# Optimization experiments

Measured on AMD Instinct MI355X. Metric: run time of the kernel, lower is better.

## Reference

```python
import jax, jax.numpy as jnp
import numpy as np
from jax import lax

B, C, H, W = 16, 512, 16, 300
K, G = 8, 2          # k_clusters, g_clusters (gvlad)
OUT = 5994           # n speakers
DN = ('NCHW', 'OIHW', 'NCHW')


def setup_inputs() -> dict:
    key = jax.random.key(0)
    ks = jax.random.split(key, 10)
    s = lambda fan: 1.0 / np.sqrt(fan)
    return {
        'x5': jax.random.normal(ks[0], (B, C, H, W), jnp.float32),
        'x4': jnp.zeros((1, 1, 1, 1), jnp.float32),
        'x3': jnp.zeros((1, 1, 1, 1), jnp.float32),
        'x2': jnp.zeros((1, 1, 1, 1), jnp.float32),
        'x1': jnp.zeros((1, 1, 1, 1), jnp.float32),
        'conv_w': jax.random.normal(ks[1], (C, C, 7, 1), jnp.float32) * s(C * 7),
        'conv_b': jnp.zeros((C,), jnp.float32),
        'cc_w': jax.random.normal(ks[2], (K + G, C, 7, 1), jnp.float32) * s(C * 7),
        'cc_b': jnp.zeros((K + G,), jnp.float32),
        'centroids': jax.random.normal(ks[3], (K + G, C), jnp.float32),
        'fc_w': jax.random.normal(ks[4], (C, C * K), jnp.float32) * s(C * K),
        'fc_b': jnp.zeros((C,), jnp.float32),
        'logit_w': jax.random.normal(ks[5], (OUT, C), jnp.float32) * s(C),
    }


def _conv(x, w, b=None):
    y = lax.conv_general_dilated(x, w, (1, 1), 'VALID', dimension_numbers=DN)
    if b is not None:
        y = y + b[None, :, None, None]
    return y


def _forward(x5, conv_w, conv_b, cc_w, cc_b, centroids, fc_w, fc_b, logit_w):
    feats = jnp.maximum(_conv(x5, conv_w, conv_b), 0.0)      # (B,C,H',W) relu conv
    scores = _conv(x5, cc_w, cc_b)                           # (B,K+G,H',W)
    assign = jax.nn.softmax(scores, axis=1)                  # soft cluster assignment
    # VLAD: sum_hw a[b,k,h,w]*(f[b,c,h,w] - cent[k,c]), computed without
    # materializing the (B,K+G,C,H',W) residual tensor (same math, fused form)
    agg = jnp.einsum('bkhw,bchw->bkc', assign, feats)        # (B,K+G,C)
    asum = jnp.sum(assign, axis=(2, 3))                      # (B,K+G)
    cluster_res = agg - asum[:, :, None] * centroids[None]   # (B,K+G,C)
    cluster_res = cluster_res[:, :K, :]                      # gvlad: drop ghost clusters
    norm = jnp.linalg.norm(cluster_res, axis=-1, keepdims=True)
    cluster_l2 = cluster_res / jnp.maximum(norm, 1e-12)
    vlad = cluster_l2.reshape(-1, K * C)                     # (B, K*C)
    emb = jnp.maximum(vlad @ fc_w.T + fc_b, 0.0)             # (B,C)
    logit = emb @ logit_w.T                                  # (B,OUT)
    return emb, logit


def reference(x5, x4, x3, x2, x1, conv_w, conv_b, cc_w, cc_b, centroids,
              fc_w, fc_b, logit_w):
    # x4..x1 are unused by Decoder.forward (only x5 flows through)
    return _forward(x5, conv_w, conv_b, cc_w, cc_b, centroids, fc_w, fc_b, logit_w)
```

## Files before the change

kernel.cpp:

```cpp
#include <hip/hip_runtime.h>
#include <hip/hip_bf16.h>

typedef __attribute__((ext_vector_type(8))) short bf16x8;
typedef __attribute__((ext_vector_type(4))) float f32x4;

__device__ __forceinline__ void async16(const void* g, void* l) {
    __builtin_amdgcn_global_load_lds(
        (const __attribute__((address_space(1))) unsigned int*)g,
        (__attribute__((address_space(3))) unsigned int*)l, 16, 0, 0);
}

__global__ __launch_bounds__(256) void pack_all(const float* __restrict__ x5,
                                                const float* __restrict__ conv_w,
                                                const float* __restrict__ cc_w,
                                                __hip_bfloat16* __restrict__ X3,
                                                __hip_bfloat16* __restrict__ A2f) {
    __shared__ __align__(16) float smem[64 * 65];
    const int f = blockIdx.x;
    if (f < 10240) {
        float(*tile)[65] = (float(*)[65])smem;
        const int ct = f / 1280, r = f % 1280;
        const int wt = r >> 8, bh = r & 255;
        const int b = bh >> 4, h = bh & 15;
        const int w0 = wt * 64, c0 = ct * 64;
        const int lw = (threadIdx.x & 15) * 4;
        const int lc = threadIdx.x >> 4;
#pragma unroll
        for (int i = 0; i < 4; ++i) {
            const int c = lc + i * 16;
            const int w = w0 + lw;
            const float* src = &x5[((size_t)(b * 512 + c0 + c) * 16 + h) * 300 + w];
            float4 v = {0.f, 0.f, 0.f, 0.f};
            if (w + 3 < 300) v = *(const float4*)src;
            else {
                if (w < 300)     v.x = src[0];
                if (w + 1 < 300) v.y = src[1];
                if (w + 2 < 300) v.z = src[2];
            }
            *(float4*)&tile[c][lw] = v;
        }
        __syncthreads();
        const int sc = (threadIdx.x & 7) * 8;
        const int sw0 = threadIdx.x >> 3;
#pragma unroll
        for (int i = 0; i < 2; ++i) {
            const int wl = sw0 + i * 32;
            const int w = w0 + wl;
            if (w < 300) {
                __hip_bfloat16 p[8];
#pragma unroll
                for (int j = 0; j < 8; ++j) p[j] = __float2bfloat16(tile[sc + j][wl]);
                *(uint4*)&X3[(((size_t)(b * 16 + h) * 300 + w)) * 512 + c0 + sc] = *(uint4*)p;
            }
        }
    } else {
        float* w = smem;
        const int co = f - 10240;
        if (co < 522) {
            const float4* src = (co < 512) ? (const float4*)(conv_w + (size_t)co * 3584)
                                           : (const float4*)(cc_w + (size_t)(co - 512) * 3584);
            for (int i = threadIdx.x; i < 896; i += 256) *(float4*)&w[i * 4] = src[i];
        } else {
            for (int i = threadIdx.x; i < 3584; i += 256) w[i] = 0.f;
        }
        __syncthreads();
        const int g = co >> 4, fl = co & 15;
        for (int chunk = threadIdx.x; chunk < 448; chunk += 256) {
            const int kk0 = chunk * 8;
            const int kt = kk0 >> 5, sq = (kk0 >> 3) & 3;
            __hip_bfloat16 p[8];
#pragma unroll
            for (int j = 0; j < 8; ++j) {
                const int k = kk0 + j;
                p[j] = __float2bfloat16(w[(k & 511) * 7 + (k >> 9)]);
            }
            char* dst = (char*)A2f + (((size_t)g * 112 + kt) * 64 + sq * 16 + fl) * 16;
            *(uint4*)dst = *(uint4*)p;
        }
    }
}

__global__ __launch_bounds__(256) void scores_gemm(
    const __hip_bfloat16* __restrict__ A2f, const __hip_bfloat16* __restrict__ X3,
    const float* __restrict__ cc_b, float* __restrict__ assign,
    float* __restrict__ asum_part, float* __restrict__ agg) {
    __shared__ __align__(16) char lds[65536];
    __shared__ float sred[4][4][4];
    const int tid = threadIdx.x;
    const int wv = tid >> 6;
    const int lane = tid & 63;
    const int gid = blockIdx.x;
    const int xcd = gid & 7;
    const int j = gid >> 3;
    const int b = xcd * 2 + (j >= 12 ? 1 : 0);
    const int nt2 = j % 12;

    {
        const int base = gid * 427;
        for (int i = tid; i < 427; i += 256) {
            const int idx = base + i;
            if (idx < 81920) agg[idx] = 0.f;
        }
    }

    const int row0 = wv * 16 + (lane >> 2);
    const int kseg = (lane & 3) ^ ((lane >> 3) & 3);
    const char* gB[4];
#pragma unroll
    for (int q = 0; q < 4; ++q) {
        int n = nt2 * 256 + row0 + q * 64;
        if (n > 2999) n = 2999;
        gB[q] = (const char*)X3 + ((size_t)((b * 16 + n / 300) * 300 + n % 300)) * 1024 + (size_t)kseg * 16;
    }
    char* lB = lds + wv * 1024 + lane * 16;

    const int wn = wv * 64;
    const int fl = lane & 15;
    const int sq = lane >> 4;
    int boff[4];
#pragma unroll
    for (int i = 0; i < 4; ++i) {
        const int swz = (sq ^ ((fl >> 1) & 3)) * 16;
        boff[i] = (wn + i * 16 + fl) * 64 + swz;
    }
    const char* Af = (const char*)A2f + (((size_t)32 * 112) << 10) + (lane << 4);

    f32x4 acc[4] = {};
    bf16x8 aC[2], aN[2];

#define S_ISSUE(ktp, ph)                                                               \
    {                                                                                  \
        const int kt0 = (ktp) * 2;                                                     \
        const size_t ba0 = (size_t)(kt0 >> 4) * 307200 + (size_t)(kt0 & 15) * 64;      \
        const size_t ba1 = (size_t)((kt0 + 1) >> 4) * 307200 + (size_t)((kt0 + 1) & 15) * 64; \
        _Pragma("unroll")                                                              \
        for (int q = 0; q < 4; ++q) {                                                  \
            async16(gB[q] + ba0, lB + (ph) * 32768 + q * 4096);                        \
            async16(gB[q] + ba1, lB + (ph) * 32768 + 16384 + q * 4096);                \
        }                                                                              \
    }
#define S_PREA(ktp, arr)                                                               \
    {                                                                                  \
        arr[0] = *(const bf16x8*)(Af + ((size_t)((ktp) * 2) << 10));                   \
        arr[1] = *(const bf16x8*)(Af + ((size_t)((ktp) * 2 + 1) << 10));               \
    }
#define S_COMP(ph, arr)                                                                \
    {                                                                                  \
        _Pragma("unroll")                                                              \
        for (int kk = 0; kk < 2; ++kk) {                                               \
            _Pragma("unroll")                                                          \
            for (int ni = 0; ni < 4; ++ni) {                                           \
                const bf16x8 bv = *(const bf16x8*)(lds + (ph) * 32768 + kk * 16384 + boff[ni]); \
                acc[ni] = __builtin_amdgcn_mfma_f32_16x16x32_bf16(arr[kk], bv, acc[ni], 0, 0, 0); \
            }                                                                          \
        }                                                                              \
    }

    S_ISSUE(0, 0);
    S_PREA(0, aC);
    for (int ktp = 0; ktp < 56; ktp += 2) {
        __syncthreads();
        S_ISSUE(ktp + 1, 1);
        S_PREA(ktp + 1, aN);
        S_COMP(0, aC);
        __syncthreads();
        if (ktp < 54) { S_ISSUE(ktp + 2, 0); S_PREA(ktp + 2, aC); }
        S_COMP(1, aN);
    }
#undef S_ISSUE
#undef S_PREA
#undef S_COMP

    float pa[4] = {0.f, 0.f, 0.f, 0.f};
#pragma unroll
    for (int ni = 0; ni < 4; ++ni) {
        const int n = nt2 * 256 + wn + ni * 16 + fl;
        const bool nval = (n < 3000);
        float s[4];
#pragma unroll
        for (int r = 0; r < 4; ++r) {
            const int k = sq * 4 + r;
            s[r] = (k < 10) ? (acc[ni][r] + cc_b[k]) : -1e30f;
        }
        float mx = fmaxf(fmaxf(s[0], s[1]), fmaxf(s[2], s[3]));
        mx = fmaxf(mx, __shfl_xor(mx, 16, 64));
        mx = fmaxf(mx, __shfl_xor(mx, 32, 64));
        float e[4], es = 0.f;
#pragma unroll
        for (int r = 0; r < 4; ++r) {
            e[r] = (sq * 4 + r < 10) ? __expf(s[r] - mx) : 0.f;
            es += e[r];
        }
        es += __shfl_xor(es, 16, 64);
        es += __shfl_xor(es, 32, 64);
        const float inv = 1.f / es;
#pragma unroll
        for (int r = 0; r < 4; ++r) {
            const int k = sq * 4 + r;
            const float a = e[r] * inv;
            if (nval) {
                if (k < 10) assign[(size_t)(b * 10 + k) * 3000 + n] = a;
                pa[r] += a;
            }
        }
    }
#pragma unroll
    for (int off = 1; off < 16; off <<= 1)
#pragma unroll
        for (int r = 0; r < 4; ++r) pa[r] += __shfl_xor(pa[r], off, 64);
    if (fl == 0) {
#pragma unroll
        for (int r = 0; r < 4; ++r) sred[wv][sq][r] = pa[r];
    }
    __syncthreads();
    if (tid < 10)
        asum_part[(nt2 * 16 + b) * 10 + tid] =
            sred[0][tid >> 2][tid & 3] + sred[1][tid >> 2][tid & 3] +
            sred[2][tid >> 2][tid & 3] + sred[3][tid >> 2][tid & 3];
}

__global__ __launch_bounds__(256, 4) void conv_gemm(
    const __hip_bfloat16* __restrict__ A2f, const __hip_bfloat16* __restrict__ X3,
    const float* __restrict__ conv_b, const float* __restrict__ assign,
    float* __restrict__ agg) {
    __shared__ __align__(16) char lds[16384];
    const int tid = threadIdx.x;
    const int wv = tid >> 6;
    const int lane = tid & 63;

    const int gid = blockIdx.x;
    const int xcd = gid & 7;
    const int j = gid >> 3;
    const int nb = xcd * 48 + (j >> 2);
    const int m0 = (j & 3) * 128;
    const int b = nb / 24;
    const int nt = nb % 24;

    const int row0 = wv * 16 + (lane >> 2);
    const int kseg = (lane & 3) ^ ((lane >> 3) & 3);
    int n0 = nt * 128 + row0;      if (n0 > 2999) n0 = 2999;
    int n1 = nt * 128 + row0 + 64; if (n1 > 2999) n1 = 2999;
    const char* gB0 = (const char*)X3 + ((size_t)((b * 16 + n0 / 300) * 300 + n0 % 300)) * 1024 + (size_t)kseg * 16;
    const char* gB1 = (const char*)X3 + ((size_t)((b * 16 + n1 / 300) * 300 + n1 % 300)) * 1024 + (size_t)kseg * 16;
    char* lB = lds + wv * 1024 + lane * 16;

    const int wm = (wv & 1) * 64;
    const int wn = (wv >> 1) * 64;
    const int fl = lane & 15;
    const int sq = lane >> 4;
    int boff[4];
#pragma unroll
    for (int i = 0; i < 4; ++i) {
        const int swz = (sq ^ ((fl >> 1) & 3)) * 16;
        boff[i] = (wn + i * 16 + fl) * 64 + swz;
    }
    const char* Af = (const char*)A2f;
    const int gb = (m0 >> 4) + ((wv & 1) << 2);

    f32x4 acc[4][4] = {};
    bf16x8 aC[4], aN[4];

#define ISSUE_B(kt, ph)                                                                \
    {                                                                                  \
        const size_t badd = (size_t)((kt) >> 4) * 307200 + (size_t)((kt) & 15) * 64;   \
        async16(gB0 + badd, lB + (ph) * 8192);                                         \
        async16(gB1 + badd, lB + (ph) * 8192 + 4096);                                  \
    }
#define PRE_A(kt, arr)                                                                 \
    {                                                                                  \
        _Pragma("unroll")                                                              \
        for (int mi = 0; mi < 4; ++mi)                                                 \
            arr[mi] = *(const bf16x8*)(Af + (((size_t)(gb + mi) * 112 + (kt)) << 10) + (lane << 4)); \
    }
#define COMPUTE(ph, arr)                                                               \
    {                                                                                  \
        _Pragma("unroll")                                                              \
        for (int ni = 0; ni < 4; ++ni) {                                               \
            const bf16x8 bv = *(const bf16x8*)(lds + (ph) * 8192 + boff[ni]);          \
            _Pragma("unroll")                                                          \
            for (int mi = 0; mi < 4; ++mi)                                             \
                acc[mi][ni] = __builtin_amdgcn_mfma_f32_16x16x32_bf16(arr[mi], bv, acc[mi][ni], 0, 0, 0); \
        }                                                                              \
    }

    ISSUE_B(0, 0);
    PRE_A(0, aC);
    for (int kt = 0; kt < 112; kt += 2) {
        __syncthreads();
        ISSUE_B(kt + 1, 1);
        PRE_A(kt + 1, aN);
        COMPUTE(0, aC);
        __syncthreads();
        if (kt < 110) { ISSUE_B(kt + 2, 0); PRE_A(kt + 2, aC); }
        COMPUTE(1, aN);
    }
#undef ISSUE_B
#undef PRE_A
#undef COMPUTE

    const int quad4 = sq * 4;
#pragma unroll
    for (int mi = 0; mi < 4; ++mi) {
        const int cob = m0 + wm + mi * 16 + quad4;
        const float b0 = conv_b[cob + 0], b1 = conv_b[cob + 1],
                    b2 = conv_b[cob + 2], b3 = conv_b[cob + 3];
#pragma unroll
        for (int ni = 0; ni < 4; ++ni) {
            acc[mi][ni][0] = fmaxf(acc[mi][ni][0] + b0, 0.f);
            acc[mi][ni][1] = fmaxf(acc[mi][ni][1] + b1, 0.f);
            acc[mi][ni][2] = fmaxf(acc[mi][ni][2] + b2, 0.f);
            acc[mi][ni][3] = fmaxf(acc[mi][ni][3] + b3, 0.f);
        }
    }
    int nn[4];
#pragma unroll
    for (int ni = 0; ni < 4; ++ni) nn[ni] = nt * 128 + wn + ni * 16 + fl;
    const float* asg = assign + (size_t)b * 30000;
    for (int k = 0; k < 10; ++k) {
        float av[4];
#pragma unroll
        for (int ni = 0; ni < 4; ++ni)
            av[ni] = (nn[ni] < 3000) ? asg[(size_t)k * 3000 + nn[ni]] : 0.f;
        float part[16];
#pragma unroll
        for (int mi = 0; mi < 4; ++mi)
#pragma unroll
            for (int r = 0; r < 4; ++r)
                part[mi * 4 + r] = av[0] * acc[mi][0][r] + av[1] * acc[mi][1][r]
                                 + av[2] * acc[mi][2][r] + av[3] * acc[mi][3][r];
#pragma unroll
        for (int off = 1; off < 16; off <<= 1)
#pragma unroll
            for (int i = 0; i < 16; ++i)
                part[i] += __shfl_xor(part[i], off, 64);
        if (fl == 0) {
            float* ag = agg + (size_t)(b * 10 + k) * 512;
#pragma unroll
            for (int mi = 0; mi < 4; ++mi)
#pragma unroll
                for (int r = 0; r < 4; ++r)
                    atomicAdd(&ag[m0 + wm + mi * 16 + quad4 + r], part[mi * 4 + r]);
        }
    }
}

__global__ __launch_bounds__(256) void fc_fused(const float* __restrict__ agg,
                                                const float* __restrict__ asum_part,
                                                const float* __restrict__ centroids,
                                                const float* __restrict__ fc_w,
                                                const float* __restrict__ fc_b,
                                                float* __restrict__ out) {
    __shared__ float res[4096];
    __shared__ float sasum[8];
    __shared__ float red[4][8];
    __shared__ float scale[8];
    const int b = blockIdx.y;
    const int t = threadIdx.x;
    if (t < 8) {
        float s = 0.f;
#pragma unroll
        for (int p = 0; p < 12; ++p) s += asum_part[(p * 16 + b) * 10 + t];
        sasum[t] = s;
    }
    __syncthreads();
    float sq[8];
#pragma unroll
    for (int k = 0; k < 8; ++k) sq[k] = 0.f;
#pragma unroll
    for (int jj = 0; jj < 16; ++jj) {
        const int i = t + jj * 256;
        const int k = jj >> 1;
        const int c = i & 511;
        const float r = agg[(size_t)(b * 10 + k) * 512 + c] - sasum[k] * centroids[k * 512 + c];
        res[i] = r;
        sq[k] += r * r;
    }
    const int lane = t & 63, w = t >> 6;
#pragma unroll
    for (int k = 0; k < 8; ++k) {
        float v = sq[k];
        for (int off = 32; off; off >>= 1) v += __shfl_xor(v, off, 64);
        if (lane == 0) red[w][k] = v;
    }
    __syncthreads();
    if (t < 8) {
        const float nrm = sqrtf(red[0][t] + red[1][t] + red[2][t] + red[3][t]);
        scale[t] = 1.f / fmaxf(nrm, 1e-12f);
    }
    __syncthreads();

    const int col = t >> 3;
    const int ks = t & 7;
    const int co = blockIdx.x * 32 + col;
    const float4* w4 = (const float4*)(fc_w + (size_t)co * 4096);
    float acc = 0.f;
    for (int i = ks; i < 1024; i += 8) {
        const float4 wv = w4[i];
        const float4 rv = *(const float4*)&res[i * 4];
        acc += (rv.x * wv.x + rv.y * wv.y + rv.z * wv.z + rv.w * wv.w) * scale[i >> 7];
    }
    acc += __shfl_down(acc, 4, 8);
    acc += __shfl_down(acc, 2, 8);
    acc += __shfl_down(acc, 1, 8);
    if (ks == 0) out[b * 512 + co] = fmaxf(acc + fc_b[co], 0.f);
}

__global__ __launch_bounds__(256) void logit_kernel(const float* __restrict__ emb,
                                                    const float* __restrict__ logit_w,
                                                    float* __restrict__ out) {
    __shared__ float se[512];
    const int gid = blockIdx.x;
    const int xcd = gid & 7;
    const int j = gid >> 3;
    const int otile = xcd * 3 + (j >> 4);
    const int b = j & 15;
    se[threadIdx.x] = emb[b * 512 + threadIdx.x];
    se[threadIdx.x + 256] = emb[b * 512 + threadIdx.x + 256];
    __syncthreads();
    const int o = otile * 256 + threadIdx.x;
    if (o < 5994) {
        const float4* w4 = (const float4*)(logit_w + (size_t)o * 512);
        float acc = 0.f;
        for (int i = 0; i < 128; ++i) {
            const float4 w = w4[i];
            acc += w.x * se[4 * i] + w.y * se[4 * i + 1] + w.z * se[4 * i + 2] + w.w * se[4 * i + 3];
        }
        out[8192 + b * 5994 + o] = acc;
    }
}

extern "C" void kernel_launch(void* const* d_in, const int* in_sizes, int n_in,
                              void* d_out, int out_size, void* d_ws, size_t ws_size,
                              hipStream_t stream) {
    (void)in_sizes; (void)n_in; (void)out_size; (void)ws_size;
    const float* x5       = (const float*)d_in[0];
    const float* conv_w   = (const float*)d_in[5];
    const float* conv_b   = (const float*)d_in[6];
    const float* cc_w     = (const float*)d_in[7];
    const float* cc_b     = (const float*)d_in[8];
    const float* centroids= (const float*)d_in[9];
    const float* fc_w     = (const float*)d_in[10];
    const float* fc_b     = (const float*)d_in[11];
    const float* logit_w  = (const float*)d_in[12];
    float* out = (float*)d_out;

    char* ws = (char*)d_ws;
    __hip_bfloat16* X3  = (__hip_bfloat16*)(ws);
    __hip_bfloat16* A2f = (__hip_bfloat16*)(ws + 78643200);
    float* assign       = (float*)(ws + 83230720);
    float* asum_part    = (float*)(ws + 85150720);
    float* agg          = (float*)(ws + 85158400);

    pack_all<<<dim3(10880), 256, 0, stream>>>(x5, conv_w, cc_w, X3, A2f);
    scores_gemm<<<dim3(192), 256, 0, stream>>>(A2f, X3, cc_b, assign, asum_part, agg);
    conv_gemm<<<dim3(1536), 256, 0, stream>>>(A2f, X3, conv_b, assign, agg);
    fc_fused<<<dim3(16, 16), 256, 0, stream>>>(agg, asum_part, centroids, fc_w, fc_b, out);
    logit_kernel<<<dim3(384), 256, 0, stream>>>(out, logit_w, out);
}
```

Measured before the change: 652.2 us.

## Shrink scores GEMM tiles to 64 columns and use a transpose-reduce for agg

The scores GEMM now runs 768 blocks of 64 columns instead of 192 blocks of 256. Each wave computes one 16x16 MFMA tile and reads its operands straight from global memory, with no LDS staging or double buffering. The aim is more parallelism across CUs for this small-K-output GEMM, at the cost of losing data reuse through LDS. In conv_gemm, the per-cluster 16-value butterfly reduction becomes a recursive-halving transpose-reduce, so each lane ends up holding one output. The two wave-halves are then combined through LDS, which cuts shuffles and atomics by a factor of two or more; asum_part and the workspace offsets are resized to match.

```diff
diff --git a/kernel.cpp b/kernel.cpp
--- a/kernel.cpp
+++ b/kernel.cpp
@@ -84,125 +84,65 @@
     const __hip_bfloat16* __restrict__ A2f, const __hip_bfloat16* __restrict__ X3,
     const float* __restrict__ cc_b, float* __restrict__ assign,
     float* __restrict__ asum_part, float* __restrict__ agg) {
-    __shared__ __align__(16) char lds[65536];
     __shared__ float sred[4][4][4];
     const int tid = threadIdx.x;
     const int wv = tid >> 6;
     const int lane = tid & 63;
+    const int fl = lane & 15;
+    const int sq = lane >> 4;
     const int gid = blockIdx.x;
     const int xcd = gid & 7;
     const int j = gid >> 3;
-    const int b = xcd * 2 + (j >= 12 ? 1 : 0);
-    const int nt2 = j % 12;
+    const int b = xcd * 2 + (j >= 48 ? 1 : 0);
+    const int nt = j % 48;
 
     {
-        const int base = gid * 427;
-        for (int i = tid; i < 427; i += 256) {
+        const int base = gid * 107;
+        for (int i = tid; i < 107; i += 256) {
             const int idx = base + i;
             if (idx < 81920) agg[idx] = 0.f;
         }
     }
 
-    const int row0 = wv * 16 + (lane >> 2);
-    const int kseg = (lane & 3) ^ ((lane >> 3) & 3);
-    const char* gB[4];
-#pragma unroll
-    for (int q = 0; q < 4; ++q) {
-        int n = nt2 * 256 + row0 + q * 64;
-        if (n > 2999) n = 2999;
-        gB[q] = (const char*)X3 + ((size_t)((b * 16 + n / 300) * 300 + n % 300)) * 1024 + (size_t)kseg * 16;
-    }
-    char* lB = lds + wv * 1024 + lane * 16;
-
-    const int wn = wv * 64;
-    const int fl = lane & 15;
-    const int sq = lane >> 4;
-    int boff[4];
-#pragma unroll
-    for (int i = 0; i < 4; ++i) {
-        const int swz = (sq ^ ((fl >> 1) & 3)) * 16;
-        boff[i] = (wn + i * 16 + fl) * 64 + swz;
-    }
-    const char* Af = (const char*)A2f + (((size_t)32 * 112) << 10) + (lane << 4);
-
-    f32x4 acc[4] = {};
-    bf16x8 aC[2], aN[2];
-
-#define S_ISSUE(ktp, ph)                                                               \
-    {                                                                                  \
-        const int kt0 = (ktp) * 2;                                                     \
-        const size_t ba0 = (size_t)(kt0 >> 4) * 307200 + (size_t)(kt0 & 15) * 64;      \
-        const size_t ba1 = (size_t)((kt0 + 1) >> 4) * 307200 + (size_t)((kt0 + 1) & 15) * 64; \
-        _Pragma("unroll")                                                              \
-        for (int q = 0; q < 4; ++q) {                                                  \
-            async16(gB[q] + ba0, lB + (ph) * 32768 + q * 4096);                        \
-            async16(gB[q] + ba1, lB + (ph) * 32768 + 16384 + q * 4096);                \
-        }                                                                              \
-    }
-#define S_PREA(ktp, arr)                                                               \
-    {                                                                                  \
-        arr[0] = *(const bf16x8*)(Af + ((size_t)((ktp) * 2) << 10));                   \
-        arr[1] = *(const bf16x8*)(Af + ((size_t)((ktp) * 2 + 1) << 10));               \
-    }
-#define S_COMP(ph, arr)                                                                \
-    {                                                                                  \
-        _Pragma("unroll")                                                              \
-        for (int kk = 0; kk < 2; ++kk) {                                               \
-            _Pragma("unroll")                                                          \
-            for (int ni = 0; ni < 4; ++ni) {                                           \
-                const bf16x8 bv = *(const bf16x8*)(lds + (ph) * 32768 + kk * 16384 + boff[ni]); \
-                acc[ni] = __builtin_amdgcn_mfma_f32_16x16x32_bf16(arr[kk], bv, acc[ni], 0, 0, 0); \
-            }                                                                          \
-        }                                                                              \
-    }
-
-    S_ISSUE(0, 0);
-    S_PREA(0, aC);
-    for (int ktp = 0; ktp < 56; ktp += 2) {
-        __syncthreads();
-        S_ISSUE(ktp + 1, 1);
-        S_PREA(ktp + 1, aN);
-        S_COMP(0, aC);
-        __syncthreads();
-        if (ktp < 54) { S_ISSUE(ktp + 2, 0); S_PREA(ktp + 2, aC); }
-        S_COMP(1, aN);
-    }
-#undef S_ISSUE
-#undef S_PREA
-#undef S_COMP
-
-    float pa[4] = {0.f, 0.f, 0.f, 0.f};
-#pragma unroll
-    for (int ni = 0; ni < 4; ++ni) {
-        const int n = nt2 * 256 + wn + ni * 16 + fl;
-        const bool nval = (n < 3000);
-        float s[4];
-#pragma unroll
-        for (int r = 0; r < 4; ++r) {
-            const int k = sq * 4 + r;
-            s[r] = (k < 10) ? (acc[ni][r] + cc_b[k]) : -1e30f;
-        }
-        float mx = fmaxf(fmaxf(s[0], s[1]), fmaxf(s[2], s[3]));
-        mx = fmaxf(mx, __shfl_xor(mx, 16, 64));
-        mx = fmaxf(mx, __shfl_xor(mx, 32, 64));
-        float e[4], es = 0.f;
-#pragma unroll
-        for (int r = 0; r < 4; ++r) {
-            e[r] = (sq * 4 + r < 10) ? __expf(s[r] - mx) : 0.f;
-            es += e[r];
-        }
-        es += __shfl_xor(es, 16, 64);
-        es += __shfl_xor(es, 32, 64);
-        const float inv = 1.f / es;
-#pragma unroll
-        for (int r = 0; r < 4; ++r) {
-            const int k = sq * 4 + r;
-            const float a = e[r] * inv;
-            if (nval) {
-                if (k < 10) assign[(size_t)(b * 10 + k) * 3000 + n] = a;
-                pa[r] += a;
-            }
-        }
+    const int n = nt * 64 + wv * 16 + fl;
+    const int nc = n > 2999 ? 2999 : n;
+    const char* gB = (const char*)X3 + ((size_t)(b * 4800 + nc)) * 1024 + sq * 16;
+    const char* Af = (const char*)A2f + (((size_t)32 * 112) << 10) + ((size_t)lane << 4);
+
+    f32x4 acc = {};
+#pragma unroll 4
+    for (int kt = 0; kt < 112; ++kt) {
+        const bf16x8 a  = *(const bf16x8*)(Af + ((size_t)kt << 10));
+        const bf16x8 bv = *(const bf16x8*)(gB + (size_t)(kt >> 4) * 307200 + (size_t)(kt & 15) * 64);
+        acc = __builtin_amdgcn_mfma_f32_16x16x32_bf16(a, bv, acc, 0, 0, 0);
+    }
+
+    float s[4];
+#pragma unroll
+    for (int r = 0; r < 4; ++r) {
+        const int k = sq * 4 + r;
+        s[r] = (k < 10) ? (acc[r] + cc_b[k]) : -1e30f;
+    }
+    float mx = fmaxf(fmaxf(s[0], s[1]), fmaxf(s[2], s[3]));
+    mx = fmaxf(mx, __shfl_xor(mx, 16, 64));
+    mx = fmaxf(mx, __shfl_xor(mx, 32, 64));
+    float e[4], es = 0.f;
+#pragma unroll
+    for (int r = 0; r < 4; ++r) {
+        e[r] = (sq * 4 + r < 10) ? __expf(s[r] - mx) : 0.f;
+        es += e[r];
+    }
+    es += __shfl_xor(es, 16, 64);
+    es += __shfl_xor(es, 32, 64);
+    const float inv = 1.f / es;
+    const bool nval = (n < 3000);
+    float pa[4];
+#pragma unroll
+    for (int r = 0; r < 4; ++r) {
+        const int k = sq * 4 + r;
+        const float a = e[r] * inv;
+        pa[r] = nval ? a : 0.f;
+        if (nval && k < 10) assign[(size_t)(b * 10 + k) * 3000 + n] = a;
     }
 #pragma unroll
     for (int off = 1; off < 16; off <<= 1)
@@ -214,7 +154,7 @@
     }
     __syncthreads();
     if (tid < 10)
-        asum_part[(nt2 * 16 + b) * 10 + tid] =
+        asum_part[(nt * 16 + b) * 10 + tid] =
             sred[0][tid >> 2][tid & 3] + sred[1][tid >> 2][tid & 3] +
             sred[2][tid >> 2][tid & 3] + sred[3][tid >> 2][tid & 3];
 }
@@ -316,6 +256,9 @@
 #pragma unroll
     for (int ni = 0; ni < 4; ++ni) nn[ni] = nt * 128 + wn + ni * 16 + fl;
     const float* asg = assign + (size_t)b * 30000;
+    const int s_ = ((fl & 1) << 3) | ((fl & 2) << 1) | ((fl & 4) >> 1) | ((fl & 8) >> 3);
+    const int co_off = (s_ >> 2) * 16 + quad4 + (s_ & 3);
+    float red10[10];
     for (int k = 0; k < 10; ++k) {
         float av[4];
 #pragma unroll
@@ -329,17 +272,31 @@
                 part[mi * 4 + r] = av[0] * acc[mi][0][r] + av[1] * acc[mi][1][r]
                                  + av[2] * acc[mi][2][r] + av[3] * acc[mi][3][r];
 #pragma unroll
-        for (int off = 1; off < 16; off <<= 1)
-#pragma unroll
-            for (int i = 0; i < 16; ++i)
-                part[i] += __shfl_xor(part[i], off, 64);
-        if (fl == 0) {
-            float* ag = agg + (size_t)(b * 10 + k) * 512;
-#pragma unroll
-            for (int mi = 0; mi < 4; ++mi)
-#pragma unroll
-                for (int r = 0; r < 4; ++r)
-                    atomicAdd(&ag[m0 + wm + mi * 16 + quad4 + r], part[mi * 4 + r]);
+        for (int bit = 0; bit < 4; ++bit) {
+            const int off = 1 << bit;
+            const int h = 8 >> bit;
+            const bool hi = (fl >> bit) & 1;
+#pragma unroll
+            for (int jj = 0; jj < h; ++jj) {
+                const float mine = hi ? part[jj + h] : part[jj];
+                const float send = hi ? part[jj] : part[jj + h];
+                part[jj] = mine + __shfl_xor(send, off, 64);
+            }
+        }
+        red10[k] = part[0];
+    }
+    float* sagg = (float*)lds;
+    if (wv < 2) {
+#pragma unroll
+        for (int k = 0; k < 10; ++k) sagg[((wv * 10 + k) << 6) + co_off] = red10[k];
+    }
+    __syncthreads();
+    if (wv >= 2) {
+        const int wmh = wv & 1;
+#pragma unroll
+        for (int k = 0; k < 10; ++k) {
+            const float v = red10[k] + sagg[((wmh * 10 + k) << 6) + co_off];
+            atomicAdd(&agg[(size_t)(b * 10 + k) * 512 + m0 + wm + co_off], v);
         }
     }
 }
@@ -359,7 +316,7 @@
     if (t < 8) {
         float s = 0.f;
 #pragma unroll
-        for (int p = 0; p < 12; ++p) s += asum_part[(p * 16 + b) * 10 + t];
+        for (int p = 0; p < 48; ++p) s += asum_part[(p * 16 + b) * 10 + t];
         sasum[t] = s;
     }
     __syncthreads();
@@ -449,10 +406,10 @@
     __hip_bfloat16* A2f = (__hip_bfloat16*)(ws + 78643200);
     float* assign       = (float*)(ws + 83230720);
     float* asum_part    = (float*)(ws + 85150720);
-    float* agg          = (float*)(ws + 85158400);
+    float* agg          = (float*)(ws + 85181440);
 
     pack_all<<<dim3(10880), 256, 0, stream>>>(x5, conv_w, cc_w, X3, A2f);
-    scores_gemm<<<dim3(192), 256, 0, stream>>>(A2f, X3, cc_b, assign, asum_part, agg);
+    scores_gemm<<<dim3(768), 256, 0, stream>>>(A2f, X3, cc_b, assign, asum_part, agg);
     conv_gemm<<<dim3(1536), 256, 0, stream>>>(A2f, X3, conv_b, assign, agg);
     fc_fused<<<dim3(16, 16), 256, 0, stream>>>(agg, asum_part, centroids, fc_w, fc_b, out);
     logit_kernel<<<dim3(384), 256, 0, stream>>>(out, logit_w, out);
```

Measured after the change: 603.3 us. -7.5%, faster.
